# Performance work log

Measured on AMD Instinct MI355X. Metric: run time of the kernel, lower is better.

## Reference

```python
import jax, jax.numpy as jnp
import numpy as np

B, C, H, W, NA = 2, 512, 25, 25, 9
A = H * W * NA  # 5625 anchors
PROB_T = 0.5
OVL_T = 0.5


def _make_anchors():
    ys, xs = np.meshgrid(np.arange(H), np.arange(W), indexing='ij')
    cx = (xs + 0.5) / W
    cy = (ys + 0.5) / H
    boxes = []
    for s in (0.1, 0.2, 0.4):
        for r in (0.5, 1.0, 2.0):
            w = s * np.sqrt(r)
            h = s / np.sqrt(r)
            boxes.append(np.stack([cx - w / 2, cy - h / 2, cx + w / 2, cy + h / 2], -1))
    anc = np.stack(boxes, axis=2)  # [H, W, 9, 4] matches [B,H,W,9*4] reshape order
    return jnp.asarray(anc.reshape(-1, 4), jnp.float32)


def setup_inputs() -> dict:
    key = jax.random.key(0)
    ks = jax.random.split(key, 4)
    x = jax.random.normal(ks[0], (B, C, H, W), jnp.float32)
    conv_w = jax.random.normal(ks[1], (512, 512, 3, 3), jnp.float32) * (1.0 / np.sqrt(512 * 9))
    conv_b = jnp.zeros((512,), jnp.float32)
    reg_w = jax.random.normal(ks[2], (36, 512), jnp.float32) * 0.02
    reg_b = jnp.zeros((36,), jnp.float32)
    cls_w = jax.random.normal(ks[3], (9, 512), jnp.float32) * 0.05
    cls_b = jnp.zeros((9,), jnp.float32)
    anchors = _make_anchors()
    return {"x": x, "conv_w": conv_w, "conv_b": conv_b, "reg_w": reg_w,
            "reg_b": reg_b, "cls_w": cls_w, "cls_b": cls_b, "anchors": anchors}


def reference(x, conv_w, conv_b, reg_w, reg_b, cls_w, cls_b, anchors):
    # --- RPN forward ---
    h = jax.lax.conv_general_dilated(x, conv_w, (1, 1), 'SAME',
                                     dimension_numbers=('NCHW', 'OIHW', 'NCHW'))
    h = jax.nn.relu(h + conv_b[None, :, None, None])
    box = jnp.einsum('bchw,oc->bhwo', h, reg_w) + reg_b  # [B,H,W,36] (== permute NHWC)
    cls = jnp.einsum('bchw,oc->bhwo', h, cls_w) + cls_b  # [B,H,W,9]
    offsets = box.reshape(B, A, 4)
    logits = cls.reshape(B, A)
    # --- detect: sigmoid + threshold ---
    probs = jax.nn.sigmoid(logits)
    valid = probs > PROB_T
    # --- box decode: gcxgcy -> cxcy -> xy (SSD-style, anchors given in xy) ---
    a_cx = (anchors[:, 0] + anchors[:, 2]) * 0.5
    a_cy = (anchors[:, 1] + anchors[:, 3]) * 0.5
    a_w = anchors[:, 2] - anchors[:, 0]
    a_h = anchors[:, 3] - anchors[:, 1]
    cx = offsets[..., 0] * a_w / 10.0 + a_cx
    cy = offsets[..., 1] * a_h / 10.0 + a_cy
    bw = jnp.exp(offsets[..., 2] / 5.0) * a_w
    bh = jnp.exp(offsets[..., 3] / 5.0) * a_h
    boxes = jnp.stack([cx - bw / 2, cy - bh / 2, cx + bw / 2, cy + bh / 2], -1)  # [B,A,4]
    # --- sort descending by score; invalid anchors sorted last and pre-suppressed ---
    sort_key = jnp.where(valid, probs, -1.0)
    order = jnp.argsort(-sort_key, axis=-1)
    sb = jnp.take_along_axis(boxes, order[..., None], axis=1)  # sorted boxes
    ss = jnp.take_along_axis(probs, order, axis=1)             # sorted scores
    sv = jnp.take_along_axis(valid, order, axis=1)             # sorted validity

    def per_image(b, v):
        x1, y1, x2, y2 = b[:, 0], b[:, 1], b[:, 2], b[:, 3]
        area = (x2 - x1) * (y2 - y1)
        iw = jnp.clip(jnp.minimum(x2[:, None], x2[None, :]) - jnp.maximum(x1[:, None], x1[None, :]), 0.0)
        ih = jnp.clip(jnp.minimum(y2[:, None], y2[None, :]) - jnp.maximum(y1[:, None], y1[None, :]), 0.0)
        inter = iw * ih
        ov = inter / (area[:, None] + area[None, :] - inter)  # [A,A] Jaccard
        sup0 = (~v).astype(jnp.int32)  # invalid anchors never considered

        def body(i, sup):
            cand = jnp.maximum(sup, (ov[i] > OVL_T).astype(jnp.int32)).at[i].set(0)
            return jnp.where(sup[i] > 0, sup, cand)  # skip if already suppressed

        sup = jax.lax.fori_loop(0, A, body, sup0)
        return (1 - sup) * v.astype(jnp.int32)

    keep = jax.vmap(per_image)(sb, sv)  # [B,A] 1 = kept detection
    return jnp.concatenate([sb, ss[..., None], keep[..., None].astype(jnp.float32)], -1)  # [B,A,6]
```

## Files before the change

### kernel.cpp

```cpp
#include <hip/hip_runtime.h>
#include <cstdint>
#include <cstddef>

#define AA 5625
#define MROWS 5696
#define NMS_DEPTH 32

__global__ __launch_bounds__(256) void k_wt(const float* __restrict__ cw,
                                            float* __restrict__ wt,
                                            int* __restrict__ Vcnt) {
  if (blockIdx.x == 0 && threadIdx.x < 2) Vcnt[threadIdx.x] = 0;
  __shared__ float t[64][65];
  int kb = (blockIdx.x % 72) * 64;
  int ob = (blockIdx.x / 72) * 64;
  int col = threadIdx.x & 63;
  int rr  = threadIdx.x >> 6;
#pragma unroll
  for (int it = 0; it < 16; ++it) {
    int row = rr + it * 4;
    t[row][col] = cw[(size_t)(ob + row) * 4608 + kb + col];
  }
  __syncthreads();
#pragma unroll
  for (int it = 0; it < 16; ++it) {
    int row = rr + it * 4;
    wt[(size_t)(kb + row) * 512 + ob + col] = t[col][row];
  }
}

__global__ void k_xpad(const float* __restrict__ x, float* __restrict__ xp) {
  int n = blockIdx.x * 256 + threadIdx.x;
  if (n >= 884736) return;
  int c = n & 31;
  int r = (n >> 5) % 27;
  int rest = (n >> 5) / 27;
  float v = 0.f;
  int oy = r - 1, ox = c - 1;
  if (oy >= 0 && oy < 25 && ox >= 0 && ox < 25)
    v = x[(size_t)rest * 625 + oy * 25 + ox];
  xp[n] = v;
}

__global__ __launch_bounds__(256) void k_conv(const float* __restrict__ wt,
                                              const float* __restrict__ xp,
                                              double* __restrict__ hpart,
                                              int Kper) {
  int cpx = gridDim.x >> 3;
  int flat = blockIdx.x;
  int logical = (flat & 7) * cpx + (flat >> 3);
  int sharer = logical % 10;
  int s      = logical / 10;
  int Nt = s & 3;
  int ks = s >> 2;
  int b  = sharer / 5;
  int Mt = sharer % 5;

  int tid = threadIdx.x;
  int m0  = Mt * 128;
  int oc0 = Nt * 128;

  int R  = (tid >> 6) * 32 + ((tid >> 4) & 3) * 8;
  int cb = 2 * (tid & 15);

  __shared__ __align__(16) double As[18][128];
  __shared__ __align__(16) double Bs[18][128];

  double acc[8][8];
#pragma unroll
  for (int i = 0; i < 8; ++i)
#pragma unroll
    for (int j = 0; j < 8; ++j) acc[i][j] = 0.0;

  int kbase = ks * Kper;
  int nchunk = Kper / 18;

  for (int ch = 0; ch < nchunk; ++ch) {
    int k0 = kbase + ch * 18;
    int ic00 = k0 / 9;
    __syncthreads();
#pragma unroll
    for (int s2 = tid; s2 < 2304; s2 += 256) {
      int row = s2 >> 7, col = s2 & 127;
      Bs[row][col] = (double)wt[(size_t)(k0 + row) * 512 + oc0 + col];
    }
#pragma unroll
    for (int s2 = tid; s2 < 2304; s2 += 256) {
      int row = s2 >> 7, col = s2 & 127;
      int m = m0 + col;
      double v = 0.0;
      if (m < 625) {
        int icl = (row >= 9) ? 1 : 0;
        int tap = row - 9 * icl;
        int dy = tap / 3, dx = tap - 3 * dy;
        int yy = m / 25, xx = m - yy * 25;
        v = (double)xp[((size_t)(b * 512 + ic00 + icl) * 27 + yy + dy) * 32 + xx + dx];
      }
      As[row][col] = v;
    }
    __syncthreads();
#pragma unroll 2
    for (int kk = 0; kk < 18; ++kk) {
      double ad[8], bd[8];
#pragma unroll
      for (int t = 0; t < 4; ++t) {
        double2 v = *(const double2*)&As[kk][R + 2 * t];
        ad[2 * t] = v.x; ad[2 * t + 1] = v.y;
      }
#pragma unroll
      for (int r = 0; r < 4; ++r) {
        double2 v = *(const double2*)&Bs[kk][cb + 32 * r];
        bd[2 * r] = v.x; bd[2 * r + 1] = v.y;
      }
#pragma unroll
      for (int i = 0; i < 8; ++i)
#pragma unroll
        for (int j = 0; j < 8; ++j) acc[i][j] += ad[i] * bd[j];
    }
  }

  double* hb = hpart + ((size_t)(ks * 2 + b) * 625) * 512 + oc0 + cb;
#pragma unroll
  for (int i = 0; i < 8; ++i) {
    int mm = m0 + R + i;
    if (mm < 625) {
      double* p = hb + (size_t)mm * 512;
#pragma unroll
      for (int r = 0; r < 4; ++r) {
        double2 v; v.x = acc[i][2 * r]; v.y = acc[i][2 * r + 1];
        *(double2*)(p + 32 * r) = v;
      }
    }
  }
}

__device__ __forceinline__ double shfl_down_d(double x, int off) {
  long long v = __double_as_longlong(x);
  int lo = __shfl_down((int)(unsigned int)(v & 0xffffffffLL), off);
  int hi = __shfl_down((int)(v >> 32), off);
  return __longlong_as_double(((long long)hi << 32) | (unsigned int)lo);
}

__global__ __launch_bounds__(256) void k_heads(
    const double* __restrict__ hpart, const float* __restrict__ conv_b,
    const float* __restrict__ reg_w, const float* __restrict__ reg_b,
    const float* __restrict__ cls_w, const float* __restrict__ cls_b,
    const float* __restrict__ anchors, float* __restrict__ boxesraw,
    float* __restrict__ probs, unsigned long long* __restrict__ keys,
    unsigned int* __restrict__ rank, int nsplit) {
  int pos = blockIdx.x % 625;
  int b   = blockIdx.x / 625;
  int tid = threadIdx.x;
  __shared__ double hv[512];
  __shared__ double res[45];
  for (int c = tid; c < 512; c += 256) {
    double s = 0.0;
    for (int k = 0; k < nsplit; ++k)
      s += hpart[(((size_t)k * 2 + b) * 625 + pos) * 512 + c];
    s += (double)conv_b[c];
    hv[c] = s > 0.0 ? s : 0.0;
  }
  __syncthreads();
  int wv = tid >> 6, l = tid & 63;
  for (int o = wv; o < 45; o += 4) {
    const float* wrow = (o < 36) ? (reg_w + (size_t)o * 512)
                                 : (cls_w + (size_t)(o - 36) * 512);
    double s = 0.0;
#pragma unroll
    for (int kk = 0; kk < 8; ++kk)
      s += hv[l + kk * 64] * (double)wrow[l + kk * 64];
#pragma unroll
    for (int d = 32; d > 0; d >>= 1) s += shfl_down_d(s, d);
    if (l == 0) res[o] = s + (double)((o < 36) ? reg_b[o] : cls_b[o - 36]);
  }
  __syncthreads();
  if (tid < 9) {
    int na = tid;
    int a = pos * 9 + na;
    double o0 = res[na * 4 + 0], o1 = res[na * 4 + 1];
    double o2 = res[na * 4 + 2], o3 = res[na * 4 + 3];
    double logit = res[36 + na];
    float4 anc = *(const float4*)(anchors + (size_t)a * 4);
    double a_cx = ((double)anc.x + (double)anc.z) * 0.5;
    double a_cy = ((double)anc.y + (double)anc.w) * 0.5;
    double a_w = (double)anc.z - (double)anc.x;
    double a_h = (double)anc.w - (double)anc.y;
    double cx = o0 * a_w / 10.0 + a_cx;
    double cy = o1 * a_h / 10.0 + a_cy;
    double bw = exp(o2 / 5.0) * a_w;
    double bh = exp(o3 / 5.0) * a_h;
    float4 box = make_float4((float)(cx - bw / 2.0), (float)(cy - bh / 2.0),
                             (float)(cx + bw / 2.0), (float)(cy + bh / 2.0));
    size_t ga = (size_t)b * AA + a;
    *(float4*)(boxesraw + ga * 4) = box;
    float p = (float)(1.0 / (1.0 + exp(-logit)));
    probs[ga] = p;
    bool valid = p > 0.5f;
    float f = -(valid ? p : -1.0f);
    unsigned int u = __float_as_uint(f);
    u = (u & 0x80000000u) ? ~u : (u | 0x80000000u);
    keys[ga] = (((unsigned long long)u) << 32) | (unsigned int)a;
    rank[ga] = 0u;
  }
}

__global__ __launch_bounds__(256) void k_count(
    const unsigned long long* __restrict__ keys, unsigned int* __restrict__ rank) {
  int b = blockIdx.z;
  int i = blockIdx.x * 256 + threadIdx.x;
  __shared__ unsigned long long sj[1024];
  unsigned long long my = (i < AA) ? keys[(size_t)b * AA + i] : 0ULL;
  int j0 = blockIdx.y * 1024;
  for (int jj = threadIdx.x; jj < 1024; jj += 256) {
    int j = j0 + jj;
    sj[jj] = (j < AA) ? keys[(size_t)b * AA + j] : ~0ULL;
  }
  __syncthreads();
  int cnt = 0;
#pragma unroll 8
  for (int jj = 0; jj < 1024; ++jj) cnt += (sj[jj] < my) ? 1 : 0;
  if (i < AA && cnt) atomicAdd(&rank[(size_t)b * AA + i], (unsigned)cnt);
}

__global__ void k_perm(const unsigned long long* __restrict__ keys,
                       const unsigned int* __restrict__ rank,
                       unsigned int* __restrict__ perm, int* __restrict__ Vcnt) {
  int idx = blockIdx.x * 256 + threadIdx.x;
  if (idx >= 2 * AA) return;
  int b = idx / AA, i = idx - b * AA;
  unsigned long long k = keys[idx];
  unsigned int r = rank[idx];
  perm[(size_t)b * AA + r] = (unsigned)i;
  if (!(k >> 63)) atomicAdd(&Vcnt[b], 1);
}

__global__ void k_assembly(const unsigned int* __restrict__ perm,
                           const float* __restrict__ boxesraw,
                           const float* __restrict__ probs,
                           float* __restrict__ out, float4* __restrict__ sb4) {
  int idx = blockIdx.x * 256 + threadIdx.x;
  if (idx >= 2 * AA) return;
  int b = idx / AA;
  unsigned int pa = perm[idx];
  float4 bx = *(const float4*)(boxesraw + ((size_t)b * AA + pa) * 4);
  float p = probs[(size_t)b * AA + pa];
  float* o = out + (size_t)idx * 6;
  o[0] = bx.x; o[1] = bx.y; o[2] = bx.z; o[3] = bx.w; o[4] = p; o[5] = 0.f;
  sb4[idx] = bx;
}

__global__ __launch_bounds__(256) void k_maskT(const float4* __restrict__ sb4,
                                               const int* __restrict__ Vcnt,
                                               ulonglong2* __restrict__ maskT) {
  int b = blockIdx.y;
  int V = Vcnt[b];
  int i = blockIdx.x * 4 + (threadIdx.x >> 6);
  if (i >= V) return;
  int lane = threadIdx.x & 63;
  float4 bif = sb4[(size_t)b * AA + i];
  double bix = bif.x, biy = bif.y, biz = bif.z, biw = bif.w;
  double ai = (biz - bix) * (biw - biy);
  unsigned long long lo = 0, hi = 0;
#pragma unroll 4
  for (int w = 0; w < 88; ++w) {
    int j = w * 64 + lane;
    int jc = (j < AA) ? j : (AA - 1);
    float4 c = sb4[(size_t)b * AA + jc];
    double aj = ((double)c.z - (double)c.x) * ((double)c.w - (double)c.y);
    double iw = fmin(biz, (double)c.z) - fmax(bix, (double)c.x);
    double ih = fmin(biw, (double)c.w) - fmax(biy, (double)c.y);
    iw = iw > 0.0 ? iw : 0.0;
    ih = ih > 0.0 ? ih : 0.0;
    double inter = iw * ih;
    double ov = inter / (ai + aj - inter);
    bool bit = (ov > 0.5) && (j != i) && (j < AA);
    unsigned long long bb = bit ? 1ULL : 0ULL;
    if (w < 64) lo |= bb << w;
    else        hi |= bb << (w - 64);
  }
  ulonglong2 v; v.x = lo; v.y = hi;
  maskT[((size_t)b * MROWS + i) * 64 + lane] = v;
}

__global__ __launch_bounds__(64) void k_nms(const ulonglong2* __restrict__ maskT,
                                            const int* __restrict__ Vcnt,
                                            float* __restrict__ out) {
  int b = blockIdx.x;
  int lane = threadIdx.x;
  int V = Vcnt[b];
  const ulonglong2* mt = maskT + (size_t)b * MROWS * 64;
  unsigned long long colLo = 0, colHi = 0;
  unsigned long long supw = 0;
  ulonglong2 ring[NMS_DEPTH];
#pragma unroll
  for (int j = 0; j < NMS_DEPTH; ++j) ring[j] = mt[(size_t)j * 64 + lane];
  for (int base = 0; base < V; base += NMS_DEPTH) {
#pragma unroll
    for (int j = 0; j < NMS_DEPTH; ++j) {
      int i = base + j;
      ulonglong2 nx = mt[(size_t)(i + NMS_DEPTH) * 64 + lane];
      if (i < V) {
        int w = i >> 6;
        int t = i & 63;
        if (t == 0)
          supw = __ballot((int)(((w < 64) ? (colLo >> w) : (colHi >> (w - 64))) & 1ULL));
        if (!((supw >> t) & 1ULL)) {
          colLo |= ring[j].x;
          colHi |= ring[j].y;
          supw = __ballot((int)(((w < 64) ? (colLo >> w) : (colHi >> (w - 64))) & 1ULL));
          if (lane == 0) out[((size_t)b * AA + i) * 6 + 5] = 1.0f;
        }
      }
      ring[j] = nx;
    }
  }
}

extern "C" void kernel_launch(void* const* d_in, const int* in_sizes, int n_in,
                              void* d_out, int out_size, void* d_ws, size_t ws_size,
                              hipStream_t stream) {
  const float* x      = (const float*)d_in[0];
  const float* conv_w = (const float*)d_in[1];
  const float* conv_b = (const float*)d_in[2];
  const float* reg_w  = (const float*)d_in[3];
  const float* reg_b  = (const float*)d_in[4];
  const float* cls_w  = (const float*)d_in[5];
  const float* cls_b  = (const float*)d_in[6];
  const float* anchors= (const float*)d_in[7];
  float* out = (float*)d_out;
  char* ws = (char*)d_ws;

  size_t off = 0;
  auto alloc = [&](size_t bytes) {
    size_t o = off;
    off += (bytes + 255) & ~(size_t)255;
    return o;
  };
  size_t o_wt   = alloc(4608ULL * 512 * 4);
  size_t o_xp   = alloc(884736ULL * 4);
  size_t o_box  = alloc(2ULL * AA * 4 * 4);
  size_t o_prob = alloc(2ULL * AA * 4);
  size_t o_keys = alloc(2ULL * AA * 8);
  size_t o_rank = alloc(2ULL * AA * 4);
  size_t o_perm = alloc(2ULL * AA * 4);
  size_t o_sb4  = alloc(2ULL * AA * 16);
  size_t o_V    = alloc(256);
  size_t o_maskT= alloc(2ULL * MROWS * 64 * 16);
  size_t fixed = off;

  int nsplit = 1;
  const int cands[5] = {16, 8, 4, 2, 1};
  for (int ci = 0; ci < 5; ++ci) {
    size_t need = fixed + (size_t)cands[ci] * 2 * 625 * 512 * 8;
    if (need <= ws_size) { nsplit = cands[ci]; break; }
  }
  size_t o_hp = alloc((size_t)nsplit * 2 * 625 * 512 * 8);

  float* wtp   = (float*)(ws + o_wt);
  float* xpp   = (float*)(ws + o_xp);
  float* boxp  = (float*)(ws + o_box);
  float* probp = (float*)(ws + o_prob);
  unsigned long long* keysp = (unsigned long long*)(ws + o_keys);
  unsigned int* rankp = (unsigned int*)(ws + o_rank);
  unsigned int* permp = (unsigned int*)(ws + o_perm);
  float4* sb4p = (float4*)(ws + o_sb4);
  int* Vp      = (int*)(ws + o_V);
  ulonglong2* maskTp = (ulonglong2*)(ws + o_maskT);
  double* hpp  = (double*)(ws + o_hp);

  k_wt<<<dim3(576), dim3(256), 0, stream>>>(conv_w, wtp, Vp);
  k_xpad<<<dim3(3456), dim3(256), 0, stream>>>(x, xpp);
  k_conv<<<dim3(40 * nsplit), dim3(256), 0, stream>>>(wtp, xpp, hpp, 4608 / nsplit);
  k_heads<<<dim3(1250), dim3(256), 0, stream>>>(hpp, conv_b, reg_w, reg_b,
                                                cls_w, cls_b, anchors, boxp,
                                                probp, keysp, rankp, nsplit);
  k_count<<<dim3(22, 6, 2), dim3(256), 0, stream>>>(keysp, rankp);
  k_perm<<<dim3(44), dim3(256), 0, stream>>>(keysp, rankp, permp, Vp);
  k_assembly<<<dim3(44), dim3(256), 0, stream>>>(permp, boxp, probp, out, sb4p);
  k_maskT<<<dim3(1407, 2), dim3(256), 0, stream>>>(sb4p, Vp, maskTp);
  k_nms<<<dim3(2), dim3(64), 0, stream>>>(maskTp, Vp, out);
}
```

Before: 643.3 us.

## Double-buffer conv tiles in fp32 LDS, drop IoU divide, batch NMS mask prefetch

The conv GEMM now keeps its tiles in LDS as floats in two buffers. Each next chunk is prefetched into registers using precomputed offsets while the current chunk is multiplied, and values are converted to double at use. This halves LDS footprint and traffic and hides global latency, but adds barriers and register pressure. The IoU test becomes a division-free comparison, and the NMS ring is restructured into two alternating prefetch banks so mask loads for later rows are issued in batches.

```diff
diff --git a/kernel.cpp b/kernel.cpp
--- a/kernel.cpp
+++ b/kernel.cpp
@@ -3,8 +3,8 @@
 #include <cstddef>
 
 #define AA 5625
-#define MROWS 5696
-#define NMS_DEPTH 32
+#define MROWS 5760
+#define ND 24
 
 __global__ __launch_bounds__(256) void k_wt(const float* __restrict__ cw,
                                             float* __restrict__ wt,
@@ -58,12 +58,11 @@
   int tid = threadIdx.x;
   int m0  = Mt * 128;
   int oc0 = Nt * 128;
-
   int R  = (tid >> 6) * 32 + ((tid >> 4) & 3) * 8;
   int cb = 2 * (tid & 15);
 
-  __shared__ __align__(16) double As[18][128];
-  __shared__ __align__(16) double Bs[18][128];
+  __shared__ __align__(16) float As[2][18][128];
+  __shared__ __align__(16) float Bs[2][18][128];
 
   double acc[8][8];
 #pragma unroll
@@ -74,47 +73,74 @@
   int kbase = ks * Kper;
   int nchunk = Kper / 18;
 
+  int ldso[9];
+  int boff[9];
+  int aoff[9];
+#pragma unroll
+  for (int t = 0; t < 9; ++t) {
+    int s2 = tid + 256 * t;
+    int row = s2 >> 7, col = s2 & 127;
+    ldso[t] = row * 128 + col;
+    boff[t] = row * 512 + oc0 + col;
+    int m = m0 + col;
+    bool av = (m < 625);
+    int mm = av ? m : 0;
+    int icl = (row >= 9) ? 1 : 0;
+    int tap = row - 9 * icl;
+    int dy = tap / 3, dx = tap - 3 * dy;
+    int yy = mm / 25, xx = mm - yy * 25;
+    int ao = (icl * 27 + yy + dy) * 32 + xx + dx;
+    aoff[t] = av ? ao : -1;
+  }
+  const float* wbase = wt + (size_t)kbase * 512;
+  const float* abase = xp + (size_t)(b * 512 + kbase / 9) * 864;
+
+  float rA[9], rB[9];
+
+#define LOADCH(CH) {                                                          \
+    int k0e = (CH) * (18 * 512);                                              \
+    int a0e = (CH) * (2 * 864);                                               \
+    _Pragma("unroll")                                                         \
+    for (int t = 0; t < 9; ++t) {                                             \
+      rB[t] = wbase[k0e + boff[t]];                                           \
+      rA[t] = (aoff[t] >= 0) ? abase[a0e + aoff[t]] : 0.f;                    \
+    } }
+#define WRITECH(BUF) {                                                        \
+    _Pragma("unroll")                                                         \
+    for (int t = 0; t < 9; ++t) {                                             \
+      ((float*)Bs[BUF])[ldso[t]] = rB[t];                                     \
+      ((float*)As[BUF])[ldso[t]] = rA[t];                                     \
+    } }
+
+  LOADCH(0);
+  WRITECH(0);
+  __syncthreads();
+
   for (int ch = 0; ch < nchunk; ++ch) {
-    int k0 = kbase + ch * 18;
-    int ic00 = k0 / 9;
-    __syncthreads();
-#pragma unroll
-    for (int s2 = tid; s2 < 2304; s2 += 256) {
-      int row = s2 >> 7, col = s2 & 127;
-      Bs[row][col] = (double)wt[(size_t)(k0 + row) * 512 + oc0 + col];
-    }
-#pragma unroll
-    for (int s2 = tid; s2 < 2304; s2 += 256) {
-      int row = s2 >> 7, col = s2 & 127;
-      int m = m0 + col;
-      double v = 0.0;
-      if (m < 625) {
-        int icl = (row >= 9) ? 1 : 0;
-        int tap = row - 9 * icl;
-        int dy = tap / 3, dx = tap - 3 * dy;
-        int yy = m / 25, xx = m - yy * 25;
-        v = (double)xp[((size_t)(b * 512 + ic00 + icl) * 27 + yy + dy) * 32 + xx + dx];
-      }
-      As[row][col] = v;
-    }
-    __syncthreads();
+    int cur = ch & 1, nxt = cur ^ 1;
+    int chn = (ch + 1 < nchunk) ? (ch + 1) : (nchunk - 1);
+    LOADCH(chn);
 #pragma unroll 2
     for (int kk = 0; kk < 18; ++kk) {
-      double ad[8], bd[8];
-#pragma unroll
-      for (int t = 0; t < 4; ++t) {
-        double2 v = *(const double2*)&As[kk][R + 2 * t];
-        ad[2 * t] = v.x; ad[2 * t + 1] = v.y;
-      }
-#pragma unroll
-      for (int r = 0; r < 4; ++r) {
-        double2 v = *(const double2*)&Bs[kk][cb + 32 * r];
-        bd[2 * r] = v.x; bd[2 * r + 1] = v.y;
-      }
+      float4 a0 = *(const float4*)&As[cur][kk][R];
+      float4 a1 = *(const float4*)&As[cur][kk][R + 4];
+      float2 b0 = *(const float2*)&Bs[cur][kk][cb];
+      float2 b1 = *(const float2*)&Bs[cur][kk][cb + 32];
+      float2 b2 = *(const float2*)&Bs[cur][kk][cb + 64];
+      float2 b3 = *(const float2*)&Bs[cur][kk][cb + 96];
+      double ad[8] = {(double)a0.x, (double)a0.y, (double)a0.z, (double)a0.w,
+                      (double)a1.x, (double)a1.y, (double)a1.z, (double)a1.w};
+      double bd[8] = {(double)b0.x, (double)b0.y, (double)b1.x, (double)b1.y,
+                      (double)b2.x, (double)b2.y, (double)b3.x, (double)b3.y};
 #pragma unroll
       for (int i = 0; i < 8; ++i)
 #pragma unroll
         for (int j = 0; j < 8; ++j) acc[i][j] += ad[i] * bd[j];
+    }
+    if (ch + 1 < nchunk) {
+      __syncthreads();
+      WRITECH(nxt);
+      __syncthreads();
     }
   }
 
@@ -131,6 +157,8 @@
       }
     }
   }
+#undef LOADCH
+#undef WRITECH
 }
 
 __device__ __forceinline__ double shfl_down_d(double x, int off) {
@@ -271,8 +299,7 @@
     iw = iw > 0.0 ? iw : 0.0;
     ih = ih > 0.0 ? ih : 0.0;
     double inter = iw * ih;
-    double ov = inter / (ai + aj - inter);
-    bool bit = (ov > 0.5) && (j != i) && (j < AA);
+    bool bit = (inter + inter > ai + aj - inter) && (j != i) && (j < AA);
     unsigned long long bb = bit ? 1ULL : 0ULL;
     if (w < 64) lo |= bb << w;
     else        hi |= bb << (w - 64);
@@ -280,6 +307,24 @@
   ulonglong2 v; v.x = lo; v.y = hi;
   maskT[((size_t)b * MROWS + i) * 64 + lane] = v;
 }
+
+#define NMS_STEP(RING, I)                                                     \
+  {                                                                           \
+    int i = (I);                                                              \
+    if (i < V) {                                                              \
+      int w = i >> 6, t = i & 63;                                             \
+      if (t == 0) {                                                           \
+        unsigned long long cbit = (w < 64) ? (colLo >> w) : (colHi >> (w - 64)); \
+        supw = __ballot((int)(cbit & 1ULL));                                  \
+      }                                                                       \
+      if (!((supw >> t) & 1ULL)) {                                            \
+        colLo |= RING.x; colHi |= RING.y;                                     \
+        unsigned long long cbit = (w < 64) ? (colLo >> w) : (colHi >> (w - 64)); \
+        supw = __ballot((int)(cbit & 1ULL));                                  \
+        if (lane == 0) out[((size_t)b * AA + i) * 6 + 5] = 1.0f;              \
+      }                                                                       \
+    }                                                                         \
+  }
 
 __global__ __launch_bounds__(64) void k_nms(const ulonglong2* __restrict__ maskT,
                                             const int* __restrict__ Vcnt,
@@ -288,32 +333,24 @@
   int lane = threadIdx.x;
   int V = Vcnt[b];
   const ulonglong2* mt = maskT + (size_t)b * MROWS * 64;
-  unsigned long long colLo = 0, colHi = 0;
-  unsigned long long supw = 0;
-  ulonglong2 ring[NMS_DEPTH];
-#pragma unroll
-  for (int j = 0; j < NMS_DEPTH; ++j) ring[j] = mt[(size_t)j * 64 + lane];
-  for (int base = 0; base < V; base += NMS_DEPTH) {
-#pragma unroll
-    for (int j = 0; j < NMS_DEPTH; ++j) {
-      int i = base + j;
-      ulonglong2 nx = mt[(size_t)(i + NMS_DEPTH) * 64 + lane];
-      if (i < V) {
-        int w = i >> 6;
-        int t = i & 63;
-        if (t == 0)
-          supw = __ballot((int)(((w < 64) ? (colLo >> w) : (colHi >> (w - 64))) & 1ULL));
-        if (!((supw >> t) & 1ULL)) {
-          colLo |= ring[j].x;
-          colHi |= ring[j].y;
-          supw = __ballot((int)(((w < 64) ? (colLo >> w) : (colHi >> (w - 64))) & 1ULL));
-          if (lane == 0) out[((size_t)b * AA + i) * 6 + 5] = 1.0f;
-        }
-      }
-      ring[j] = nx;
-    }
-  }
-}
+  unsigned long long colLo = 0, colHi = 0, supw = 0;
+  ulonglong2 ra[ND], rb[ND];
+#pragma unroll
+  for (int j = 0; j < ND; ++j) ra[j] = mt[(size_t)j * 64 + lane];
+#pragma unroll
+  for (int j = 0; j < ND; ++j) rb[j] = mt[(size_t)(ND + j) * 64 + lane];
+  for (int base = 0; base < V; base += 2 * ND) {
+#pragma unroll
+    for (int j = 0; j < ND; ++j) NMS_STEP(ra[j], base + j);
+#pragma unroll
+    for (int j = 0; j < ND; ++j) ra[j] = mt[(size_t)(base + 2 * ND + j) * 64 + lane];
+#pragma unroll
+    for (int j = 0; j < ND; ++j) NMS_STEP(rb[j], base + ND + j);
+#pragma unroll
+    for (int j = 0; j < ND; ++j) rb[j] = mt[(size_t)(base + 3 * ND + j) * 64 + lane];
+  }
+}
+#undef NMS_STEP
 
 extern "C" void kernel_launch(void* const* d_in, const int* in_sizes, int n_in,
                               void* d_out, int out_size, void* d_ws, size_t ws_size,
```

After: 545.8 us. -15.2%, faster.
